# Kernel tuning notes

Measured on AMD Instinct MI355X. Metric: run time of the kernel, lower is better.

## Reference

```python
import jax, jax.numpy as jnp
import numpy as np

B_, L_, DIN, DM, DS, DR, K = 2, 1024, 1024, 2048, 16, 128, 4


def setup_inputs() -> dict:
    key = jax.random.key(0)
    ks = jax.random.split(key, 10)
    s = lambda k, shape, sc=0.02: (jax.random.normal(k, shape, jnp.float32) * sc)
    A_init = jnp.tile(jnp.arange(1, DS + 1, dtype=jnp.float32)[None, :], (DM, 1))  # (DM, DS)
    return {
        'x_in': jax.random.normal(ks[0], (B_, L_, DIN), jnp.float32),
        'W_in': s(ks[1], (DIN, DM)),
        'W_res': s(ks[2], (DIN, DM)),
        'W_out': s(ks[3], (DM, DIN)),
        'conv_w': s(ks[4], (DM, K), 0.1),   # depthwise conv weight (torch shape (DM,1,K) squeezed)
        'conv_b': jnp.zeros((DM,), jnp.float32),
        'A_log': jnp.log(A_init),
        'D': jnp.ones((DM,), jnp.float32),
        'W_B': s(ks[5], (DM, DS)),
        'W_C': s(ks[6], (DM, DS)),
        'W_dt': s(ks[7], (DM, DR)),
        'dt_w': s(ks[8], (DR, DM)),
        'dt_b': jnp.zeros((DM,), jnp.float32),
    }


def reference(x_in, W_in, W_res, W_out, conv_w, conv_b, A_log, D, W_B, W_C, W_dt, dt_w, dt_b):
    Bb, L, _ = x_in.shape
    x = x_in @ W_in                     # (B, L, DM)
    res = x_in @ W_res                  # (B, L, DM)
    # Causal depthwise conv1d: pad left k-1, truncate to L (matches Conv1d(padding=k-1)[:, :, :L])
    xp = jnp.pad(x, ((0, 0), (K - 1, 0), (0, 0)))
    xc = conv_b
    for i in range(K):
        xc = xc + xp[:, i:i + L, :] * conv_w[:, i]
    xc = jax.nn.silu(xc)                # (B, L, DM)
    # Selective SSM (fused_ssm)
    A = -jnp.exp(A_log)                 # (DM, DS)
    Bp = xc @ W_B                       # (B, L, DS)
    Cp = xc @ W_C                       # (B, L, DS)
    delta = jax.nn.softplus((xc @ W_dt) @ dt_w + dt_b)  # (B, L, DM)
    dA = jnp.exp(delta[..., None] * A)                       # (B, L, DM, DS)
    dBu = delta[..., None] * Bp[:, :, None, :] * xc[..., None]  # (B, L, DM, DS)

    def step(h, inp):
        dA_t, dBu_t, C_t = inp
        h = dA_t * h + dBu_t                         # (B, DM, DS)
        y = jnp.einsum('bdn,bn->bd', h, C_t)         # (B, DM)
        return h, y

    h0 = jnp.zeros((Bb, DM, DS), jnp.float32)
    _, ys = jax.lax.scan(step, h0, (dA.transpose(1, 0, 2, 3), dBu.transpose(1, 0, 2, 3), Cp.transpose(1, 0, 2)))
    y = ys.transpose(1, 0, 2) + D * xc  # (B, L, DM)
    y = y * jax.nn.silu(res)
    return y @ W_out                    # (B, L, DIN)
```

## Files before the change

kernel.cpp:

```cpp
#include <hip/hip_runtime.h>
#include <hip/hip_bf16.h>

constexpr int B_  = 2;
constexpr int L_  = 1024;
constexpr int DIN = 1024;
constexpr int DM  = 2048;
constexpr int DS  = 16;
constexpr int DR  = 128;
constexpr int KC  = 4;
constexpr int M_  = B_ * L_;
constexpr int NP2 = 256;
constexpr int NPC = 160;
constexpr int KSLICES = 8;
constexpr int KSL = DM / KSLICES;

constexpr int NC = 32;
constexpr int CL = L_ / NC;
constexpr int S_ = B_ * DM * DS;

typedef __bf16 bf16x8 __attribute__((ext_vector_type(8)));
typedef __bf16 bf16x4 __attribute__((ext_vector_type(4)));
typedef float  f32x4  __attribute__((ext_vector_type(4)));

__device__ __forceinline__ void gload_lds16(const void* g, void* l) {
    __builtin_amdgcn_global_load_lds(
        (const __attribute__((address_space(1))) void*)g,
        (__attribute__((address_space(3))) void*)l, 16, 0, 0);
}

__device__ __forceinline__ void transpose_block(const float* __restrict__ in,
                                                __bf16* __restrict__ out,
                                                int R, int C, int bx, int by, int t) {
    __shared__ float tile[32][33];
    int tx = t & 31, ty = t >> 5;
    #pragma unroll
    for (int j = 0; j < 32; j += 8)
        tile[ty + j][tx] = in[(size_t)(by * 32 + ty + j) * C + (bx * 32 + tx)];
    __syncthreads();
    #pragma unroll
    for (int j = 0; j < 32; j += 8)
        out[(size_t)(bx * 32 + ty + j) * R + (by * 32 + tx)] = (__bf16)tile[tx][ty + j];
}

__global__ void prep_all(const float* __restrict__ x_in, const float* __restrict__ W_in,
                         const float* __restrict__ W_res, const float* __restrict__ W_out,
                         const float* __restrict__ dt_w,
                         const float* __restrict__ W_B, const float* __restrict__ W_C,
                         const float* __restrict__ W_dt, const float* __restrict__ conv_w,
                         __bf16* __restrict__ xinB, __bf16* __restrict__ WinT,
                         __bf16* __restrict__ WresT, __bf16* __restrict__ WoutT,
                         __bf16* __restrict__ dtwT, __bf16* __restrict__ projW,
                         float* __restrict__ cwT, float* __restrict__ outz) {
    int blk = blockIdx.x, t = threadIdx.x;
    if (blk < 2048) {
        int i4 = blk * 256 + t;
        f32x4 v = ((const f32x4*)x_in)[i4];
        bf16x4 o;
        #pragma unroll
        for (int q = 0; q < 4; q++) o[q] = (__bf16)v[q];
        ((bf16x4*)xinB)[i4] = o;
    } else if (blk < 4096) {
        int b = blk - 2048;
        transpose_block(W_in, WinT, DIN, DM, b % 64, b / 64, t);
    } else if (blk < 6144) {
        int b = blk - 4096;
        transpose_block(W_res, WresT, DIN, DM, b % 64, b / 64, t);
    } else if (blk < 8192) {
        int b = blk - 6144;
        transpose_block(W_out, WoutT, DM, DIN, b % 32, b / 32, t);
    } else if (blk < 8448) {
        int b = blk - 8192;
        transpose_block(dt_w, dtwT, DR, DM, b % 64, b / 64, t);
    } else if (blk < 10496) {
        int i = (blk - 8448) * 256 + t;
        int k = i % DM;
        int n = i / DM;
        float v = 0.f;
        if (n < 16)        v = W_B[(size_t)k * DS + n];
        else if (n < 32)   v = W_C[(size_t)k * DS + (n - 16)];
        else if (n < 160)  v = W_dt[(size_t)k * DR + (n - 32)];
        projW[i] = (__bf16)v;
    } else if (blk < 10528) {
        int j = (blk - 10496) * 256 + t;
        int tap = j / DM, d = j % DM;
        cwT[j] = conv_w[d * KC + tap];
    } else {
        int i = (blk - 10528) * 256 + t;
        ((f32x4*)outz)[i] = f32x4{0.f, 0.f, 0.f, 0.f};
    }
}

__global__ void reduce_split(const __bf16* __restrict__ PpartB, float* __restrict__ Bp,
                             float* __restrict__ Cp, __bf16* __restrict__ dtmpB) {
    int i = blockIdx.x * 256 + threadIdx.x;
    int row = i / NPC, c = i % NPC;
    float v = 0.f;
    #pragma unroll
    for (int ks = 0; ks < KSLICES; ks++)
        v += (float)PpartB[(size_t)ks * M_ * NPC + i];
    if (c < 16)       Bp[(size_t)row * DS + c] = v;
    else if (c < 32)  Cp[(size_t)row * DS + (c - 16)] = v;
    else              dtmpB[(size_t)row * DR + (c - 32)] = (__bf16)v;
}

__global__ __launch_bounds__(1024, 4)
void gemm_in_conv(const __bf16* __restrict__ A, const __bf16* __restrict__ BT,
                  __bf16* __restrict__ xcB, __bf16* __restrict__ resB,
                  const float* __restrict__ cwT, const float* __restrict__ conv_b) {
    __shared__ __bf16 smem[32768];
    const int lda = DIN, ldb = DIN, K = DIN;
    int t = threadIdx.x;
    int lane = t & 63, w = t >> 6;
    int wm = w >> 2, wn = w & 3;
    int m0 = blockIdx.y * 128, n0 = blockIdx.x * 128;
    int q = lane >> 4, rr = lane & 15;
    bool is_x = (n0 < DM);
    bool has_halo = is_x && ((m0 & (L_ - 1)) != 0);

    f32x4 acc[2][2] = {};
    f32x4 hacc[2] = {};

    const int nt = K >> 6;

    int t2 = t & 511;
    int srow = t2 >> 2;
    int slot = t2 & 3;
    int gkb = slot ^ ((srow >> 1) & 3);

    auto SA = [&](int buf, int s) { return smem + (buf * 2 + s) * 4096; };
    auto SB = [&](int buf, int s) { return smem + 16384 + (buf * 2 + s) * 4096; };

    auto stage = [&](int kt, int bufi) {
        if (t < 512) {
            #pragma unroll
            for (int s = 0; s < 2; s++)
                gload_lds16(A + (size_t)(m0 + srow) * lda + kt + s * 32 + gkb * 8,
                            SA(bufi, s) + w * 512);
        } else {
            #pragma unroll
            for (int s = 0; s < 2; s++)
                gload_lds16(BT + (size_t)(n0 + srow) * ldb + kt + s * 32 + gkb * 8,
                            SB(bufi, s) + (w - 8) * 512);
        }
    };

    bf16x8 ah[2];
    if (wm == 0 && has_halo) {
        #pragma unroll
        for (int s = 0; s < 2; s++)
            ah[s] = *(const bf16x8*)(A + (size_t)(m0 - 16 + rr) * lda + s * 32 + q * 8);
    }

    stage(0, 0);
    __syncthreads();

    int cur = 0;
    for (int tix = 0; tix < nt; tix++) {
        if (tix + 1 < nt) stage((tix + 1) << 6, cur ^ 1);

        bf16x8 ahn[2];
        if (wm == 0 && has_halo && tix + 1 < nt) {
            int ktn = (tix + 1) << 6;
            #pragma unroll
            for (int s = 0; s < 2; s++)
                ahn[s] = *(const bf16x8*)(A + (size_t)(m0 - 16 + rr) * lda + ktn + s * 32 + q * 8);
        }

        #pragma unroll
        for (int s = 0; s < 2; s++) {
            bf16x8 af[2], bfr[2];
            #pragma unroll
            for (int i = 0; i < 2; i++) {
                int rowA = wm * 32 + i * 16 + rr;
                af[i] = *(const bf16x8*)(SA(cur, s) + rowA * 32 + ((q ^ ((rowA >> 1) & 3)) * 8));
            }
            #pragma unroll
            for (int j = 0; j < 2; j++) {
                int rowB = wn * 32 + j * 16 + rr;
                bfr[j] = *(const bf16x8*)(SB(cur, s) + rowB * 32 + ((q ^ ((rowB >> 1) & 3)) * 8));
            }
            #pragma unroll
            for (int i = 0; i < 2; i++)
                #pragma unroll
                for (int j = 0; j < 2; j++)
                    acc[i][j] = __builtin_amdgcn_mfma_f32_16x16x32_bf16(af[i], bfr[j], acc[i][j], 0, 0, 0);
            if (wm == 0 && has_halo) {
                hacc[0] = __builtin_amdgcn_mfma_f32_16x16x32_bf16(ah[s], bfr[0], hacc[0], 0, 0, 0);
                hacc[1] = __builtin_amdgcn_mfma_f32_16x16x32_bf16(ah[s], bfr[1], hacc[1], 0, 0, 0);
            }
        }
        if (wm == 0 && has_halo && tix + 1 < nt) { ah[0] = ahn[0]; ah[1] = ahn[1]; }

        __syncthreads();
        cur ^= 1;
    }

    if (!is_x) {
        #pragma unroll
        for (int i = 0; i < 2; i++) {
            #pragma unroll
            for (int j = 0; j < 2; j++) {
                int col = (n0 - DM) + wn * 32 + j * 16 + rr;
                #pragma unroll
                for (int jj = 0; jj < 4; jj++) {
                    int row = m0 + wm * 32 + i * 16 + q * 4 + jj;
                    resB[(size_t)row * DM + col] = (__bf16)acc[i][j][jj];
                }
            }
        }
        return;
    }

    constexpr int XS = 136;
    #pragma unroll
    for (int i = 0; i < 2; i++)
        #pragma unroll
        for (int j = 0; j < 2; j++) {
            int cc = wn * 32 + j * 16 + rr;
            #pragma unroll
            for (int jj = 0; jj < 4; jj++) {
                int r = wm * 32 + i * 16 + q * 4 + jj;
                smem[(r + 3) * XS + cc] = (__bf16)acc[i][j][jj];
            }
        }
    if (wm == 0) {
        #pragma unroll
        for (int j = 0; j < 2; j++) {
            int cc = wn * 32 + j * 16 + rr;
            #pragma unroll
            for (int jj = 0; jj < 4; jj++) {
                int r = q * 4 + jj;
                if (r >= 13)
                    smem[(r - 13) * XS + cc] = has_halo ? (__bf16)hacc[j][jj] : (__bf16)0.f;
            }
        }
    }
    __syncthreads();

    {
        int c  = t & 127;
        int rg = t >> 7;
        int d  = n0 + c;
        float w0 = cwT[0 * DM + d], w1 = cwT[1 * DM + d];
        float w2 = cwT[2 * DM + d], w3 = cwT[3 * DM + d];
        float bv = conv_b[d];
        float x0 = (float)smem[(rg * 16 + 0) * XS + c];
        float x1 = (float)smem[(rg * 16 + 1) * XS + c];
        float x2 = (float)smem[(rg * 16 + 2) * XS + c];
        #pragma unroll
        for (int k = 0; k < 16; k++) {
            float x3 = (float)smem[(rg * 16 + k + 3) * XS + c];
            float v = fmaf(x3, w3, fmaf(x2, w2, fmaf(x1, w1, fmaf(x0, w0, bv))));
            float sv = v / (1.f + __expf(-v));
            xcB[(size_t)(m0 + rg * 16 + k) * DM + d] = (__bf16)sv;
            x0 = x1; x1 = x2; x2 = x3;
        }
    }
}

template<int EPI>
__global__ __launch_bounds__(1024, 8)
void gemm_tile128(const __bf16* __restrict__ A, const __bf16* __restrict__ BT,
                  __bf16* __restrict__ Cb, const float* __restrict__ bias,
                  int M, int N, int K, int lda, int ldb) {
    __shared__ __bf16 sA[2][2][128 * 32];
    __shared__ __bf16 sB[2][2][128 * 32];
    int t = threadIdx.x;
    int lane = t & 63, w = t >> 6;
    int wm = w >> 2, wn = w & 3;
    int m0 = blockIdx.y * 128, n0 = blockIdx.x * 128;
    int kbase = blockIdx.z * K;
    int q = lane >> 4, rr = lane & 15;

    f32x4 acc[2][2] = {};

    const int nt = K >> 6;

    int t2 = t & 511;
    int srow = t2 >> 2;
    int slot = t2 & 3;
    int gkb = slot ^ ((srow >> 1) & 3);

    auto stage = [&](int kt, int bufi) {
        if (t < 512) {
            #pragma unroll
            for (int s = 0; s < 2; s++)
                gload_lds16(A + (size_t)(m0 + srow) * lda + kbase + kt + s * 32 + gkb * 8,
                            &sA[bufi][s][w * 512]);
        } else {
            #pragma unroll
            for (int s = 0; s < 2; s++)
                gload_lds16(BT + (size_t)(n0 + srow) * ldb + kbase + kt + s * 32 + gkb * 8,
                            &sB[bufi][s][(w - 8) * 512]);
        }
    };

    stage(0, 0);
    __syncthreads();

    int cur = 0;
    for (int tix = 0; tix < nt; tix++) {
        if (tix + 1 < nt) stage((tix + 1) << 6, cur ^ 1);

        #pragma unroll
        for (int s = 0; s < 2; s++) {
            bf16x8 af[2], bfr[2];
            #pragma unroll
            for (int i = 0; i < 2; i++) {
                int rowA = wm * 32 + i * 16 + rr;
                af[i] = *(const bf16x8*)(&sA[cur][s][rowA * 32 + ((q ^ ((rowA >> 1) & 3)) * 8)]);
            }
            #pragma unroll
            for (int j = 0; j < 2; j++) {
                int rowB = wn * 32 + j * 16 + rr;
                bfr[j] = *(const bf16x8*)(&sB[cur][s][rowB * 32 + ((q ^ ((rowB >> 1) & 3)) * 8)]);
            }
            #pragma unroll
            for (int i = 0; i < 2; i++)
                #pragma unroll
                for (int j = 0; j < 2; j++)
                    acc[i][j] = __builtin_amdgcn_mfma_f32_16x16x32_bf16(af[i], bfr[j], acc[i][j], 0, 0, 0);
        }

        __syncthreads();
        cur ^= 1;
    }

    #pragma unroll
    for (int i = 0; i < 2; i++) {
        #pragma unroll
        for (int j = 0; j < 2; j++) {
            int col = n0 + wn * 32 + j * 16 + rr;
            #pragma unroll
            for (int jj = 0; jj < 4; jj++) {
                int row = m0 + wm * 32 + i * 16 + q * 4 + jj;
                float v = acc[i][j][jj];
                if (EPI == 1) {
                    float z = v + bias[col];
                    Cb[(size_t)row * N + col] = (__bf16)((z > 20.f) ? z : log1pf(__expf(z)));
                } else {
                    if (col < NPC)
                        Cb[(size_t)blockIdx.z * M * NPC + (size_t)row * NPC + col] = (__bf16)v;
                }
            }
        }
    }
}

__global__ void gemm_out64(const __bf16* __restrict__ A, const __bf16* __restrict__ BT,
                           float* __restrict__ C, int M, int N, int K, int lda, int ldb) {
    __shared__ __bf16 sA[2][2][128 * 32];
    __shared__ __bf16 sB[2][2][64 * 32];
    int t = threadIdx.x;
    int lane = t & 63, w = t >> 6;
    int wm = w >> 1, wn = w & 1;
    int m0 = blockIdx.y * 128, n0 = blockIdx.x * 64;
    int kh = K >> 1;
    int kbase = blockIdx.z * kh;
    int q = lane >> 4, rr = lane & 15;

    f32x4 acc[2][2] = {};
    int srow = t >> 2;
    int slot = t & 3;

    const int nt = kh >> 6;

    auto stage = [&](int kt, int bufi) {
        int gkb = slot ^ ((srow >> 1) & 3);
        #pragma unroll
        for (int s = 0; s < 2; s++) {
            gload_lds16(A + (size_t)(m0 + srow) * lda + kbase + kt + s * 32 + gkb * 8,
                        &sA[bufi][s][w * 512]);
            if (t < 256)
                gload_lds16(BT + (size_t)(n0 + srow) * ldb + kbase + kt + s * 32 + gkb * 8,
                            &sB[bufi][s][w * 512]);
        }
    };

    stage(0, 0);
    __syncthreads();

    int cur = 0;
    for (int tix = 0; tix < nt; tix++) {
        if (tix + 1 < nt) stage((tix + 1) << 6, cur ^ 1);

        #pragma unroll
        for (int s = 0; s < 2; s++) {
            bf16x8 af[2], bfr[2];
            #pragma unroll
            for (int i = 0; i < 2; i++) {
                int rowA = wm * 32 + i * 16 + rr;
                af[i] = *(const bf16x8*)(&sA[cur][s][rowA * 32 + ((q ^ ((rowA >> 1) & 3)) * 8)]);
            }
            #pragma unroll
            for (int j = 0; j < 2; j++) {
                int rowB = wn * 32 + j * 16 + rr;
                bfr[j] = *(const bf16x8*)(&sB[cur][s][rowB * 32 + ((q ^ ((rowB >> 1) & 3)) * 8)]);
            }
            #pragma unroll
            for (int i = 0; i < 2; i++)
                #pragma unroll
                for (int j = 0; j < 2; j++)
                    acc[i][j] = __builtin_amdgcn_mfma_f32_16x16x32_bf16(af[i], bfr[j], acc[i][j], 0, 0, 0);
        }

        __syncthreads();
        cur ^= 1;
    }

    #pragma unroll
    for (int i = 0; i < 2; i++) {
        #pragma unroll
        for (int j = 0; j < 2; j++) {
            int col = n0 + wn * 32 + j * 16 + rr;
            #pragma unroll
            for (int jj = 0; jj < 4; jj++) {
                int row = m0 + wm * 32 + i * 16 + q * 4 + jj;
                atomicAdd(&C[(size_t)row * N + col], acc[i][j][jj]);
            }
        }
    }
}

__global__ void scan_phase1(const __bf16* __restrict__ delta, const __bf16* __restrict__ xc,
                            const float* __restrict__ Bp, const float* __restrict__ A_log,
                            __bf16* __restrict__ aprodB, __bf16* __restrict__ cendB) {
    int blk = blockIdx.x;
    int c   = blk % NC;
    int rem = blk / NC;
    int dmt = rem % (DM / 256);
    int b   = rem / (DM / 256);
    int t   = threadIdx.x;
    int dm  = dmt * 256 + t;
    int l0  = c * CL;

    __shared__ float sB[CL * DS];
    sB[t]       = Bp[((size_t)b * L_ + l0) * DS + t];
    sB[t + 256] = Bp[((size_t)b * L_ + l0) * DS + t + 256];
    __syncthreads();

    float Aval[DS];
    {
        const f32x4* Ap = (const f32x4*)(A_log + (size_t)dm * DS);
        #pragma unroll
        for (int r4 = 0; r4 < 4; r4++) {
            f32x4 a = Ap[r4];
            #pragma unroll
            for (int q = 0; q < 4; q++) Aval[r4 * 4 + q] = -__expf(a[q]);
        }
    }

    float h[DS], ap[DS];
    #pragma unroll
    for (int i = 0; i < DS; i++) { h[i] = 0.f; ap[i] = 1.f; }

    size_t base = ((size_t)b * L_ + l0) * DM + dm;
    #pragma unroll 4
    for (int j = 0; j < CL; j++) {
        float dl  = (float)delta[base + (size_t)j * DM];
        float xv  = (float)xc[base + (size_t)j * DM];
        float cmn = dl * xv;
        const f32x4* sB4 = (const f32x4*)(sB + j * DS);
        #pragma unroll
        for (int r4 = 0; r4 < 4; r4++) {
            f32x4 bv = sB4[r4];
            #pragma unroll
            for (int q = 0; q < 4; q++) {
                int i = r4 * 4 + q;
                float dA = __expf(dl * Aval[i]);
                ap[i] *= dA;
                h[i] = fmaf(dA, h[i], cmn * bv[q]);
            }
        }
    }

    size_t s = ((size_t)(b * DM + dm)) * DS;
    #pragma unroll
    for (int r8 = 0; r8 < 2; r8++) {
        bf16x8 va, vh;
        #pragma unroll
        for (int q = 0; q < 8; q++) { va[q] = (__bf16)ap[r8 * 8 + q]; vh[q] = (__bf16)h[r8 * 8 + q]; }
        ((bf16x8*)(aprodB + (size_t)c * S_ + s))[r8] = va;
        ((bf16x8*)(cendB  + (size_t)c * S_ + s))[r8] = vh;
    }
}

__global__ void scan_phase2(const __bf16* __restrict__ aprodB, const __bf16* __restrict__ cendB,
                            __bf16* __restrict__ hinitB) {
    int u = blockIdx.x * 256 + threadIdx.x;
    float h = 0.f;
    #pragma unroll
    for (int c = 0; c < NC; c++) {
        float a  = (float)aprodB[(size_t)c * S_ + u];
        float ce = (float)cendB [(size_t)c * S_ + u];
        hinitB[(size_t)c * S_ + u] = (__bf16)h;
        h = fmaf(a, h, ce);
    }
}

__global__ void scan_phase3(const __bf16* __restrict__ delta, const __bf16* __restrict__ xc,
                            const float* __restrict__ Bp, const float* __restrict__ Cp,
                            const __bf16* __restrict__ res, const float* __restrict__ A_log,
                            const float* __restrict__ Dw, const __bf16* __restrict__ hinitB,
                            __bf16* __restrict__ ybar) {
    int blk = blockIdx.x;
    int c   = blk % NC;
    int rem = blk / NC;
    int dmt = rem % (DM / 256);
    int b   = rem / (DM / 256);
    int t   = threadIdx.x;
    int dm  = dmt * 256 + t;
    int l0  = c * CL;

    __shared__ float sB[CL * DS];
    __shared__ float sC[CL * DS];
    sB[t]       = Bp[((size_t)b * L_ + l0) * DS + t];
    sB[t + 256] = Bp[((size_t)b * L_ + l0) * DS + t + 256];
    sC[t]       = Cp[((size_t)b * L_ + l0) * DS + t];
    sC[t + 256] = Cp[((size_t)b * L_ + l0) * DS + t + 256];
    __syncthreads();

    float Aval[DS];
    {
        const f32x4* Ap = (const f32x4*)(A_log + (size_t)dm * DS);
        #pragma unroll
        for (int r4 = 0; r4 < 4; r4++) {
            f32x4 a = Ap[r4];
            #pragma unroll
            for (int q = 0; q < 4; q++) Aval[r4 * 4 + q] = -__expf(a[q]);
        }
    }
    float Dval = Dw[dm];

    float h[DS];
    {
        size_t s = ((size_t)(b * DM + dm)) * DS;
        #pragma unroll
        for (int r8 = 0; r8 < 2; r8++) {
            bf16x8 v = ((const bf16x8*)(hinitB + (size_t)c * S_ + s))[r8];
            #pragma unroll
            for (int q = 0; q < 8; q++) h[r8 * 8 + q] = (float)v[q];
        }
    }

    size_t base = ((size_t)b * L_ + l0) * DM + dm;
    #pragma unroll 4
    for (int j = 0; j < CL; j++) {
        float dl  = (float)delta[base + (size_t)j * DM];
        float xv  = (float)xc[base + (size_t)j * DM];
        float rv  = (float)res[base + (size_t)j * DM];
        float cmn = dl * xv;
        float y = 0.f;
        const f32x4* sB4 = (const f32x4*)(sB + j * DS);
        const f32x4* sC4 = (const f32x4*)(sC + j * DS);
        #pragma unroll
        for (int r4 = 0; r4 < 4; r4++) {
            f32x4 bv = sB4[r4];
            f32x4 cv = sC4[r4];
            #pragma unroll
            for (int q = 0; q < 4; q++) {
                int i = r4 * 4 + q;
                float dA = __expf(dl * Aval[i]);
                h[i] = fmaf(dA, h[i], cmn * bv[q]);
                y = fmaf(h[i], cv[q], y);
            }
        }
        float g = rv / (1.f + __expf(-rv));
        ybar[base + (size_t)j * DM] = (__bf16)((y + Dval * xv) * g);
    }
}

extern "C" void kernel_launch(void* const* d_in, const int* in_sizes, int n_in,
                              void* d_out, int out_size, void* d_ws, size_t ws_size,
                              hipStream_t stream) {
    const float* x_in   = (const float*)d_in[0];
    const float* W_in   = (const float*)d_in[1];
    const float* W_res  = (const float*)d_in[2];
    const float* W_out  = (const float*)d_in[3];
    const float* conv_w = (const float*)d_in[4];
    const float* conv_b = (const float*)d_in[5];
    const float* A_log  = (const float*)d_in[6];
    const float* Dw     = (const float*)d_in[7];
    const float* W_B    = (const float*)d_in[8];
    const float* W_C    = (const float*)d_in[9];
    const float* W_dt   = (const float*)d_in[10];
    const float* dt_w   = (const float*)d_in[11];
    const float* dt_b   = (const float*)d_in[12];

    float* ws_f = (float*)d_ws;
    float* Bp    = ws_f;
    float* Cp    = Bp + (size_t)M_ * DS;
    float* cwT   = Cp + (size_t)M_ * DS;
    __bf16* bf_base = (__bf16*)(cwT + (size_t)KC * DM);
    __bf16* ybar   = bf_base;
    __bf16* xinB   = ybar   + (size_t)M_ * DM;
    __bf16* WinT   = xinB   + (size_t)M_ * DIN;
    __bf16* WresT  = WinT   + (size_t)DM * DIN;
    __bf16* WoutT  = WresT  + (size_t)DM * DIN;
    __bf16* xB     = WoutT  + (size_t)DIN * DM;
    __bf16* xcB    = xB     + (size_t)M_ * DM;
    __bf16* projW  = xcB    + (size_t)M_ * DM;
    __bf16* dtwT   = projW  + (size_t)NP2 * DM;
    __bf16* dtmpB  = dtwT   + (size_t)DM * DR;
    __bf16* deltaB = dtmpB  + (size_t)M_ * DR;
    __bf16* resB   = deltaB + (size_t)M_ * DM;
    __bf16* aprodB = resB   + (size_t)M_ * DM;
    __bf16* cendB  = aprodB + (size_t)NC * S_;
    __bf16* hinitB = cendB  + (size_t)NC * S_;
    __bf16* PpartB = hinitB + (size_t)NC * S_;

    prep_all<<<12576, 256, 0, stream>>>(x_in, W_in, W_res, W_out, dt_w, W_B, W_C, W_dt,
                                        conv_w, xinB, WinT, WresT, WoutT, dtwT, projW,
                                        cwT, (float*)d_out);

    gemm_in_conv<<<dim3((2 * DM) / 128, M_ / 128), 1024, 0, stream>>>(
        xinB, WinT, xcB, resB, cwT, conv_b);

    gemm_tile128<4><<<dim3(NP2 / 128, M_ / 128, KSLICES), 1024, 0, stream>>>(
        xcB, projW, PpartB, nullptr, M_, NP2, KSL, DM, DM);
    reduce_split<<<(M_ * NPC) / 256, 256, 0, stream>>>(PpartB, Bp, Cp, dtmpB);

    gemm_tile128<1><<<dim3(DM / 128, M_ / 128, 1), 1024, 0, stream>>>(
        dtmpB, dtwT, deltaB, dt_b, M_, DM, DR, DR, DR);

    int nblk = B_ * (DM / 256) * NC;
    scan_phase1<<<nblk, 256, 0, stream>>>(deltaB, xcB, Bp, A_log, aprodB, cendB);
    scan_phase2<<<S_ / 256, 256, 0, stream>>>(aprodB, cendB, hinitB);
    scan_phase3<<<nblk, 256, 0, stream>>>(deltaB, xcB, Bp, Cp, resB, A_log, Dw, hinitB, ybar);

    gemm_out64<<<dim3(DIN / 64, M_ / 128, 2), 512, 0, stream>>>(
        ybar, WoutT, (float*)d_out, M_, DIN, DM, DM, DM);
}
```

Before: 242.0 us.

## Fold chunk-prefix scan into phase3 and vectorize transpose stores

```diff
diff --git a/kernel.cpp b/kernel.cpp
--- a/kernel.cpp
+++ b/kernel.cpp
@@ -20,6 +20,7 @@
 
 typedef __bf16 bf16x8 __attribute__((ext_vector_type(8)));
 typedef __bf16 bf16x4 __attribute__((ext_vector_type(4)));
+typedef __bf16 bf16x2 __attribute__((ext_vector_type(2)));
 typedef float  f32x4  __attribute__((ext_vector_type(4)));
 
 __device__ __forceinline__ void gload_lds16(const void* g, void* l) {
@@ -37,9 +38,12 @@
     for (int j = 0; j < 32; j += 8)
         tile[ty + j][tx] = in[(size_t)(by * 32 + ty + j) * C + (bx * 32 + tx)];
     __syncthreads();
-    #pragma unroll
-    for (int j = 0; j < 32; j += 8)
-        out[(size_t)(bx * 32 + ty + j) * R + (by * 32 + tx)] = (__bf16)tile[tx][ty + j];
+    int ox = (t & 15) * 2, oy = t >> 4;
+    #pragma unroll
+    for (int j = 0; j < 32; j += 16) {
+        bf16x2 v = {(__bf16)tile[ox][oy + j], (__bf16)tile[ox + 1][oy + j]};
+        *(bf16x2*)(out + (size_t)(bx * 32 + oy + j) * R + (by * 32 + ox)) = v;
+    }
 }
 
 __global__ void prep_all(const float* __restrict__ x_in, const float* __restrict__ W_in,
@@ -485,24 +489,11 @@
     }
 }
 
-__global__ void scan_phase2(const __bf16* __restrict__ aprodB, const __bf16* __restrict__ cendB,
-                            __bf16* __restrict__ hinitB) {
-    int u = blockIdx.x * 256 + threadIdx.x;
-    float h = 0.f;
-    #pragma unroll
-    for (int c = 0; c < NC; c++) {
-        float a  = (float)aprodB[(size_t)c * S_ + u];
-        float ce = (float)cendB [(size_t)c * S_ + u];
-        hinitB[(size_t)c * S_ + u] = (__bf16)h;
-        h = fmaf(a, h, ce);
-    }
-}
-
 __global__ void scan_phase3(const __bf16* __restrict__ delta, const __bf16* __restrict__ xc,
                             const float* __restrict__ Bp, const float* __restrict__ Cp,
                             const __bf16* __restrict__ res, const float* __restrict__ A_log,
-                            const float* __restrict__ Dw, const __bf16* __restrict__ hinitB,
-                            __bf16* __restrict__ ybar) {
+                            const float* __restrict__ Dw, const __bf16* __restrict__ aprodB,
+                            const __bf16* __restrict__ cendB, __bf16* __restrict__ ybar) {
     int blk = blockIdx.x;
     int c   = blk % NC;
     int rem = blk / NC;
@@ -532,14 +523,22 @@
     }
     float Dval = Dw[dm];
 
+    size_t s = ((size_t)(b * DM + dm)) * DS;
+
     float h[DS];
-    {
-        size_t s = ((size_t)(b * DM + dm)) * DS;
+    #pragma unroll
+    for (int i = 0; i < DS; i++) h[i] = 0.f;
+    for (int cc = 0; cc < c; cc++) {
+        const bf16x8* va = (const bf16x8*)(aprodB + (size_t)cc * S_ + s);
+        const bf16x8* vc = (const bf16x8*)(cendB  + (size_t)cc * S_ + s);
         #pragma unroll
         for (int r8 = 0; r8 < 2; r8++) {
-            bf16x8 v = ((const bf16x8*)(hinitB + (size_t)c * S_ + s))[r8];
-            #pragma unroll
-            for (int q = 0; q < 8; q++) h[r8 * 8 + q] = (float)v[q];
+            bf16x8 a = va[r8], ce = vc[r8];
+            #pragma unroll
+            for (int q = 0; q < 8; q++) {
+                int i = r8 * 8 + q;
+                h[i] = fmaf((float)a[q], h[i], (float)ce[q]);
+            }
         }
     }
 
@@ -625,8 +624,8 @@
 
     int nblk = B_ * (DM / 256) * NC;
     scan_phase1<<<nblk, 256, 0, stream>>>(deltaB, xcB, Bp, A_log, aprodB, cendB);
-    scan_phase2<<<S_ / 256, 256, 0, stream>>>(aprodB, cendB, hinitB);
-    scan_phase3<<<nblk, 256, 0, stream>>>(deltaB, xcB, Bp, Cp, resB, A_log, Dw, hinitB, ybar);
+    scan_phase3<<<nblk, 256, 0, stream>>>(deltaB, xcB, Bp, Cp, resB, A_log, Dw,
+                                          aprodB, cendB, ybar);
 
     gemm_out64<<<dim3(DIN / 64, M_ / 128, 2), 512, 0, stream>>>(
         ybar, WoutT, (float*)d_out, M_, DIN, DM, DM, DM);
```

Measured after the change: 248.7 us. 1.03x slower.
